# Performance work log

Hardware: AMD Instinct MI355X
Metric: run time of the kernel (lower is better)

Reference implementation:

```python
import jax, jax.numpy as jnp
import numpy as np

B, T, E = 2048, 200, 128
H1, H2 = 64, 32
NEG_INF = -(2.0 ** 32) + 1.0  # matches tf source's -2**32 + 1 padding value


def setup_inputs() -> dict:
    key = jax.random.key(0)
    ks = jax.random.split(key, 8)
    queries = jax.random.normal(ks[0], (B, E), dtype=jnp.float32)
    keys = jax.random.normal(ks[1], (B, T, E), dtype=jnp.float32)
    keys_id = jax.random.randint(ks[2], (B, T), 0, 2, dtype=jnp.int32)
    # Dense params: MLP input is concat([q,k,q-k,q*k]) -> 4*E = 512
    W1 = jax.random.normal(ks[3], (4 * E, H1), dtype=jnp.float32) * (1.0 / np.sqrt(4 * E))
    b1 = jnp.zeros((H1,), dtype=jnp.float32)
    W2 = jax.random.normal(ks[4], (H1, H2), dtype=jnp.float32) * (1.0 / np.sqrt(H1))
    b2 = jnp.zeros((H2,), dtype=jnp.float32)
    W3 = jax.random.normal(ks[5], (H2, 1), dtype=jnp.float32) * (1.0 / np.sqrt(H2))
    b3 = jnp.zeros((1,), dtype=jnp.float32)
    return {"queries": queries, "keys": keys, "keys_id": keys_id,
            "W1": W1, "b1": b1, "W2": W2, "b2": b2, "W3": W3, "b3": b3}


def reference(queries, keys, keys_id, W1, b1, W2, b2, W3, b3):
    # tile query over the time axis: [B,E] -> [B,T,E]
    q = jnp.broadcast_to(queries[:, None, :], keys.shape)
    # concat features: [B,T,4E]
    feat = jnp.concatenate([q, keys, q - keys, q * keys], axis=2)
    # small MLP scorer
    h = jax.nn.relu(jnp.einsum('btf,fh->bth', feat, W1) + b1)
    h = jax.nn.relu(jnp.einsum('bth,hk->btk', h, W2) + b2)
    weight = jnp.einsum('btk,ko->bto', h, W3) + b3  # [B,T,1]
    # masked softmax over time axis (padding id == 0)
    mask = (keys_id != 0)[:, :, None]  # [B,T,1]
    weight = jnp.where(mask, weight, jnp.float32(NEG_INF))
    weight = jax.nn.softmax(weight, axis=1)
    # weighted mean pooling (original uses reduce_mean, i.e. sum/T)
    return jnp.mean(weight * keys, axis=1)  # [B,E]
```

## Files before the change

### kernel.cpp

```cpp
#include <hip/hip_runtime.h>
#include <hip/hip_bf16.h>

#define NEG_INF_F (-4294967295.0f)

typedef __attribute__((ext_vector_type(8))) short bf16x8;
typedef __attribute__((ext_vector_type(4))) float f32x4;

__device__ __forceinline__ unsigned short f2bf(float x) {
    unsigned u = __float_as_uint(x);
    return (unsigned short)((u + 0x7fffu + ((u >> 16) & 1u)) >> 16);
}
__device__ __forceinline__ unsigned f2bf2(float a, float b) {
    __hip_bfloat162 h2 = __float22bfloat162_rn(make_float2(a, b));
    unsigned r; __builtin_memcpy(&r, &h2, 4); return r;
}
__device__ __forceinline__ float bf2f(unsigned short s) {
    return __uint_as_float(((unsigned)s) << 16);
}

struct __align__(16) Smem {
    unsigned short K[200 * 128];
    unsigned short h1s[4][16 * 64];
    float q[128];
    float maskf[208];
    float cpart[256];
    float s[208];
    float ppart[128];
    float red[16];
};
static_assert(sizeof(Smem) <= 64 * 1024, "LDS over 64 KiB");

__global__ __launch_bounds__(256, 2)
void attn_fused(const float* __restrict__ Q,
                const float* __restrict__ Kg,
                const int*   __restrict__ kid,
                const float* __restrict__ W1,
                const float* __restrict__ b1,
                const float* __restrict__ W2,
                const float* __restrict__ b2,
                const float* __restrict__ W3,
                const float* __restrict__ b3,
                float* __restrict__ out)
{
    __shared__ Smem sm;
    const int b    = blockIdx.x;
    const int tid  = threadIdx.x;
    const int wave = tid >> 6;
    const int lane = tid & 63;
    const int l15  = lane & 15;
    const int quad = lane >> 4;

    {
        const float4* src = reinterpret_cast<const float4*>(Kg + (size_t)b * 200 * 128);
        #pragma unroll
        for (int r = 0; r < 25; ++r) {
            const int idx4 = tid + 256 * r;
            const float4 v = src[idx4];
            const int t = idx4 >> 5;
            const int e = (idx4 & 31) << 2;
            const int g = (e >> 3) ^ (t & 15);
            uint2 pk;
            pk.x = f2bf2(v.x, v.y);
            pk.y = f2bf2(v.z, v.w);
            *reinterpret_cast<uint2*>(&sm.K[t * 128 + g * 8 + (e & 7)]) = pk;
        }
    }
    if (tid < 128) sm.q[tid] = Q[b * 128 + tid];
    if (tid < 200) sm.maskf[tid] = (kid[b * 200 + tid] != 0) ? 1.0f : 0.0f;
    __syncthreads();

    bf16x8 W2f[2][2];
    #pragma unroll
    for (int ks = 0; ks < 2; ++ks) {
        #pragma unroll
        for (int nt = 0; nt < 2; ++nt) {
            const int n = nt * 16 + l15;
            const int kb = ks * 32 + quad * 8;
            bf16x8 f;
            #pragma unroll
            for (int j = 0; j < 8; ++j) f[j] = (short)f2bf(W2[(kb + j) * 32 + n]);
            W2f[ks][nt] = f;
        }
    }
    const float w3a = W3[l15],  w3b = W3[16 + l15];
    const float b2a = b2[l15],  b2b = b2[16 + l15];
    const float b3v = b3[0];

    {
        const int n = tid & 63, kc = tid >> 6;
        float acc = (kc == 0) ? b1[n] : 0.0f;
        #pragma unroll 4
        for (int i = 0; i < 32; ++i) {
            const int k = kc * 32 + i;
            acc += sm.q[k] * (W1[k * 64 + n] + W1[(256 + k) * 64 + n]);
        }
        sm.cpart[kc * 64 + n] = acc;
    }

    bf16x8 Mf[4][4];
    {
        unsigned short* Mbuf = &sm.h1s[0][0];
        const int n   = tid & 63;
        const int w16 = (tid >> 6) * 16;
        #pragma unroll
        for (int hf = 0; hf < 2; ++hf) {
            #pragma unroll
            for (int j = 0; j < 16; j += 2) {
                const int kp = w16 + j;
                const int k  = hf * 64 + kp;
                const float v0 = (W1[(128 + k) * 64 + n] - W1[(256 + k) * 64 + n])
                               + sm.q[k] * W1[(384 + k) * 64 + n];
                const float v1 = (W1[(129 + k) * 64 + n] - W1[(257 + k) * 64 + n])
                               + sm.q[k + 1] * W1[(385 + k) * 64 + n];
                const int g = (kp >> 3) ^ (n & 7);
                *reinterpret_cast<unsigned*>(&Mbuf[n * 64 + g * 8 + (kp & 7)]) = f2bf2(v0, v1);
            }
            __syncthreads();
            #pragma unroll
            for (int ksl = 0; ksl < 2; ++ksl) {
                #pragma unroll
                for (int nt = 0; nt < 4; ++nt) {
                    const int nn = nt * 16 + l15;
                    const int g  = (ksl * 4 + quad) ^ (nn & 7);
                    Mf[hf * 2 + ksl][nt] = *reinterpret_cast<const bf16x8*>(&Mbuf[nn * 64 + g * 8]);
                }
            }
            __syncthreads();
        }
    }
    float cn[4];
    #pragma unroll
    for (int nt = 0; nt < 4; ++nt) {
        const int n = nt * 16 + l15;
        cn[nt] = sm.cpart[n] + sm.cpart[64 + n] + sm.cpart[128 + n] + sm.cpart[192 + n];
    }

    unsigned short* h1w = &sm.h1s[wave][0];
    const f32x4 zero4 = {0.f, 0.f, 0.f, 0.f};

    for (int tile = wave; tile < 13; tile += 4) {
        const int t0 = tile * 16;
        const int t  = t0 + l15;
        f32x4 acc[4] = {zero4, zero4, zero4, zero4};
        #pragma unroll
        for (int ks = 0; ks < 4; ++ks) {
            const int g = (ks * 4 + quad) ^ (t & 15);
            const bf16x8 A = *reinterpret_cast<const bf16x8*>(&sm.K[t * 128 + g * 8]);
            #pragma unroll
            for (int nt = 0; nt < 4; ++nt)
                acc[nt] = __builtin_amdgcn_mfma_f32_16x16x32_bf16(A, Mf[ks][nt], acc[nt], 0, 0, 0);
        }
        #pragma unroll
        for (int nt = 0; nt < 4; ++nt) {
            const int n = nt * 16 + l15;
            #pragma unroll
            for (int r = 0; r < 4; ++r) {
                const int m = quad * 4 + r;
                const float h = fmaxf(acc[nt][r] + cn[nt], 0.0f);
                const int g = (n >> 3) ^ (m & 7);
                h1w[m * 64 + g * 8 + (n & 7)] = f2bf(h);
            }
        }
        f32x4 p0 = zero4, p1 = zero4;
        #pragma unroll
        for (int ks = 0; ks < 2; ++ks) {
            const int g = (ks * 4 + quad) ^ (l15 & 7);
            const bf16x8 A2 = *reinterpret_cast<const bf16x8*>(&h1w[l15 * 64 + g * 8]);
            p0 = __builtin_amdgcn_mfma_f32_16x16x32_bf16(A2, W2f[ks][0], p0, 0, 0, 0);
            p1 = __builtin_amdgcn_mfma_f32_16x16x32_bf16(A2, W2f[ks][1], p1, 0, 0, 0);
        }
        float sv[4];
        #pragma unroll
        for (int r = 0; r < 4; ++r)
            sv[r] = fmaxf(p0[r] + b2a, 0.f) * w3a + fmaxf(p1[r] + b2b, 0.f) * w3b;
        #pragma unroll
        for (int off = 1; off < 16; off <<= 1) {
            #pragma unroll
            for (int r = 0; r < 4; ++r) sv[r] += __shfl_xor(sv[r], off);
        }
        if (l15 == 0) {
            #pragma unroll
            for (int r = 0; r < 4; ++r) {
                const int tt = t0 + quad * 4 + r;
                if (tt < 200)
                    sm.s[tt] = (sm.maskf[tt] != 0.0f) ? (sv[r] + b3v) : NEG_INF_F;
                else if (tt < 208)
                    sm.s[tt] = -__builtin_inff();
            }
        }
    }
    __syncthreads();

    {
        const float v = (tid < 208) ? sm.s[tid] : -__builtin_inff();
        float m = v;
        #pragma unroll
        for (int off = 32; off >= 1; off >>= 1) m = fmaxf(m, __shfl_xor(m, off));
        if (lane == 0) sm.red[wave] = m;
        __syncthreads();
        m = fmaxf(fmaxf(sm.red[0], sm.red[1]), fmaxf(sm.red[2], sm.red[3]));
        const float ev = (tid < 208) ? __expf(v - m) : 0.0f;
        float ssum = ev;
        #pragma unroll
        for (int off = 32; off >= 1; off >>= 1) ssum += __shfl_xor(ssum, off);
        if (lane == 0) sm.red[8 + wave] = ssum;
        __syncthreads();
        const float S = sm.red[8] + sm.red[9] + sm.red[10] + sm.red[11];
        const float inv = 1.0f / (S * 200.0f);
        if (tid < 208) sm.s[tid] = ev * inv;
    }
    __syncthreads();

    {
        const int e  = tid & 127;
        const int h  = tid >> 7;
        const int e3 = e & 7;
        const int eh = e >> 3;
        float a0 = 0.f, a1 = 0.f, a2 = 0.f, a3 = 0.f;
        const int tb0 = h * 100;
        #pragma unroll
        for (int i = 0; i < 25; ++i) {
            const int tb = tb0 + i * 4;
            const float4 wv = *reinterpret_cast<const float4*>(&sm.s[tb]);
            a0 += wv.x * bf2f(sm.K[(tb + 0) * 128 + ((eh ^ ((tb + 0) & 15)) * 8) + e3]);
            a1 += wv.y * bf2f(sm.K[(tb + 1) * 128 + ((eh ^ ((tb + 1) & 15)) * 8) + e3]);
            a2 += wv.z * bf2f(sm.K[(tb + 2) * 128 + ((eh ^ ((tb + 2) & 15)) * 8) + e3]);
            a3 += wv.w * bf2f(sm.K[(tb + 3) * 128 + ((eh ^ ((tb + 3) & 15)) * 8) + e3]);
        }
        const float acc2 = (a0 + a1) + (a2 + a3);
        if (h == 1) sm.ppart[e] = acc2;
        __syncthreads();
        if (h == 0) out[(size_t)b * 128 + e] = acc2 + sm.ppart[e];
    }
}

extern "C" void kernel_launch(void* const* d_in, const int* in_sizes, int n_in,
                              void* d_out, int out_size, void* d_ws, size_t ws_size,
                              hipStream_t stream) {
    (void)in_sizes; (void)n_in; (void)out_size; (void)d_ws; (void)ws_size;
    attn_fused<<<dim3(2048), dim3(256), 0, stream>>>(
        (const float*)d_in[0], (const float*)d_in[1], (const int*)d_in[2],
        (const float*)d_in[3], (const float*)d_in[4], (const float*)d_in[5],
        (const float*)d_in[6], (const float*)d_in[7], (const float*)d_in[8],
        (float*)d_out);
}
```

Baseline: 345.8 us.

## Double block size to 512 threads and redistribute all phases across eight waves

Launches 512 threads per block instead of 256 and splits every phase (K load/convert, W1 precompute, MFMA tiles, softmax reductions, weighted pooling) across eight waves, growing the LDS scratch arrays to match. The Q and mask loads are issued before the K staging loop so their latency overlaps it. More threads per block cut per-block latency, but the larger LDS footprint and the 13 tiles spread over 8 waves (uneven load) may reduce blocks per CU and occupancy.

New measurement: 352.6 us. About the same (+2.0%).

```diff
diff --git a/kernel.cpp b/kernel.cpp
--- a/kernel.cpp
+++ b/kernel.cpp
@@ -20,17 +20,17 @@
 
 struct __align__(16) Smem {
     unsigned short K[200 * 128];
-    unsigned short h1s[4][16 * 64];
+    unsigned short h1s[8][16 * 64];
     float q[128];
     float maskf[208];
-    float cpart[256];
+    float cpart[512];
     float s[208];
-    float ppart[128];
+    float ppart[384];
     float red[16];
 };
-static_assert(sizeof(Smem) <= 64 * 1024, "LDS over 64 KiB");
-
-__global__ __launch_bounds__(256, 2)
+static_assert(sizeof(Smem) <= 80 * 1024, "LDS over 80 KiB (need 2 blocks/CU)");
+
+__global__ __launch_bounds__(512, 4)
 void attn_fused(const float* __restrict__ Q,
                 const float* __restrict__ Kg,
                 const int*   __restrict__ kid,
@@ -50,11 +50,15 @@
     const int l15  = lane & 15;
     const int quad = lane >> 4;
 
+    const float qv = (tid < 128) ? Q[b * 128 + tid] : 0.0f;
+    const int   kv = (tid < 200) ? kid[b * 200 + tid] : 0;
+
     {
         const float4* src = reinterpret_cast<const float4*>(Kg + (size_t)b * 200 * 128);
         #pragma unroll
-        for (int r = 0; r < 25; ++r) {
-            const int idx4 = tid + 256 * r;
+        for (int r = 0; r < 13; ++r) {
+            const int idx4 = tid + 512 * r;
+            if (r == 12 && tid >= 256) break;
             const float4 v = src[idx4];
             const int t = idx4 >> 5;
             const int e = (idx4 & 31) << 2;
@@ -65,8 +69,8 @@
             *reinterpret_cast<uint2*>(&sm.K[t * 128 + g * 8 + (e & 7)]) = pk;
         }
     }
-    if (tid < 128) sm.q[tid] = Q[b * 128 + tid];
-    if (tid < 200) sm.maskf[tid] = (kid[b * 200 + tid] != 0) ? 1.0f : 0.0f;
+    if (tid < 128) sm.q[tid] = qv;
+    if (tid < 200) sm.maskf[tid] = (kv != 0) ? 1.0f : 0.0f;
     __syncthreads();
 
     bf16x8 W2f[2][2];
@@ -90,8 +94,8 @@
         const int n = tid & 63, kc = tid >> 6;
         float acc = (kc == 0) ? b1[n] : 0.0f;
         #pragma unroll 4
-        for (int i = 0; i < 32; ++i) {
-            const int k = kc * 32 + i;
+        for (int i = 0; i < 16; ++i) {
+            const int k = kc * 16 + i;
             acc += sm.q[k] * (W1[k * 64 + n] + W1[(256 + k) * 64 + n]);
         }
         sm.cpart[kc * 64 + n] = acc;
@@ -100,13 +104,13 @@
     bf16x8 Mf[4][4];
     {
         unsigned short* Mbuf = &sm.h1s[0][0];
-        const int n   = tid & 63;
-        const int w16 = (tid >> 6) * 16;
+        const int n  = tid & 63;
+        const int w8 = (tid >> 6) * 8;
         #pragma unroll
         for (int hf = 0; hf < 2; ++hf) {
             #pragma unroll
-            for (int j = 0; j < 16; j += 2) {
-                const int kp = w16 + j;
+            for (int j = 0; j < 8; j += 2) {
+                const int kp = w8 + j;
                 const int k  = hf * 64 + kp;
                 const float v0 = (W1[(128 + k) * 64 + n] - W1[(256 + k) * 64 + n])
                                + sm.q[k] * W1[(384 + k) * 64 + n];
@@ -132,13 +136,16 @@
     #pragma unroll
     for (int nt = 0; nt < 4; ++nt) {
         const int n = nt * 16 + l15;
-        cn[nt] = sm.cpart[n] + sm.cpart[64 + n] + sm.cpart[128 + n] + sm.cpart[192 + n];
+        float a = 0.f;
+        #pragma unroll
+        for (int kc = 0; kc < 8; ++kc) a += sm.cpart[kc * 64 + n];
+        cn[nt] = a;
     }
 
     unsigned short* h1w = &sm.h1s[wave][0];
     const f32x4 zero4 = {0.f, 0.f, 0.f, 0.f};
 
-    for (int tile = wave; tile < 13; tile += 4) {
+    for (int tile = wave; tile < 13; tile += 8) {
         const int t0 = tile * 16;
         const int t  = t0 + l15;
         f32x4 acc[4] = {zero4, zero4, zero4, zero4};
@@ -198,39 +205,46 @@
         for (int off = 32; off >= 1; off >>= 1) m = fmaxf(m, __shfl_xor(m, off));
         if (lane == 0) sm.red[wave] = m;
         __syncthreads();
-        m = fmaxf(fmaxf(sm.red[0], sm.red[1]), fmaxf(sm.red[2], sm.red[3]));
+        m = sm.red[0];
+        #pragma unroll
+        for (int w = 1; w < 8; ++w) m = fmaxf(m, sm.red[w]);
         const float ev = (tid < 208) ? __expf(v - m) : 0.0f;
         float ssum = ev;
         #pragma unroll
         for (int off = 32; off >= 1; off >>= 1) ssum += __shfl_xor(ssum, off);
         if (lane == 0) sm.red[8 + wave] = ssum;
         __syncthreads();
-        const float S = sm.red[8] + sm.red[9] + sm.red[10] + sm.red[11];
+        float S = sm.red[8];
+        #pragma unroll
+        for (int w = 1; w < 8; ++w) S += sm.red[8 + w];
         const float inv = 1.0f / (S * 200.0f);
         if (tid < 208) sm.s[tid] = ev * inv;
     }
     __syncthreads();
 
     {
-        const int e  = tid & 127;
-        const int h  = tid >> 7;
-        const int e3 = e & 7;
-        const int eh = e >> 3;
+        const int e   = tid & 127;
+        const int qtr = tid >> 7;
+        const int e3  = e & 7;
+        const int eh  = e >> 3;
+        const int tb0 = qtr * 50;
         float a0 = 0.f, a1 = 0.f, a2 = 0.f, a3 = 0.f;
-        const int tb0 = h * 100;
-        #pragma unroll
-        for (int i = 0; i < 25; ++i) {
+        #pragma unroll
+        for (int i = 0; i < 12; ++i) {
             const int tb = tb0 + i * 4;
-            const float4 wv = *reinterpret_cast<const float4*>(&sm.s[tb]);
-            a0 += wv.x * bf2f(sm.K[(tb + 0) * 128 + ((eh ^ ((tb + 0) & 15)) * 8) + e3]);
-            a1 += wv.y * bf2f(sm.K[(tb + 1) * 128 + ((eh ^ ((tb + 1) & 15)) * 8) + e3]);
-            a2 += wv.z * bf2f(sm.K[(tb + 2) * 128 + ((eh ^ ((tb + 2) & 15)) * 8) + e3]);
-            a3 += wv.w * bf2f(sm.K[(tb + 3) * 128 + ((eh ^ ((tb + 3) & 15)) * 8) + e3]);
-        }
+            a0 += sm.s[tb + 0] * bf2f(sm.K[(tb + 0) * 128 + ((eh ^ ((tb + 0) & 15)) * 8) + e3]);
+            a1 += sm.s[tb + 1] * bf2f(sm.K[(tb + 1) * 128 + ((eh ^ ((tb + 1) & 15)) * 8) + e3]);
+            a2 += sm.s[tb + 2] * bf2f(sm.K[(tb + 2) * 128 + ((eh ^ ((tb + 2) & 15)) * 8) + e3]);
+            a3 += sm.s[tb + 3] * bf2f(sm.K[(tb + 3) * 128 + ((eh ^ ((tb + 3) & 15)) * 8) + e3]);
+        }
+        const int tb = tb0 + 48;
+        a0 += sm.s[tb + 0] * bf2f(sm.K[(tb + 0) * 128 + ((eh ^ ((tb + 0) & 15)) * 8) + e3]);
+        a1 += sm.s[tb + 1] * bf2f(sm.K[(tb + 1) * 128 + ((eh ^ ((tb + 1) & 15)) * 8) + e3]);
         const float acc2 = (a0 + a1) + (a2 + a3);
-        if (h == 1) sm.ppart[e] = acc2;
+        if (qtr != 0) sm.ppart[(qtr - 1) * 128 + e] = acc2;
         __syncthreads();
-        if (h == 0) out[(size_t)b * 128 + e] = acc2 + sm.ppart[e];
+        if (qtr == 0)
+            out[(size_t)b * 128 + e] = acc2 + sm.ppart[e] + sm.ppart[128 + e] + sm.ppart[256 + e];
     }
 }
 
@@ -238,7 +252,7 @@
                               void* d_out, int out_size, void* d_ws, size_t ws_size,
                               hipStream_t stream) {
     (void)in_sizes; (void)n_in; (void)out_size; (void)d_ws; (void)ws_size;
-    attn_fused<<<dim3(2048), dim3(256), 0, stream>>>(
+    attn_fused<<<dim3(2048), dim3(512), 0, stream>>>(
         (const float*)d_in[0], (const float*)d_in[1], (const int*)d_in[2],
         (const float*)d_in[3], (const float*)d_in[4], (const float*)d_in[5],
         (const float*)d_in[6], (const float*)d_in[7], (const float*)d_in[8],
```
